# Performance work log

Measured on AMD Instinct MI355X. Metric: run time of the kernel, lower is better.

The kernel has to match this reference:

```python
import jax, jax.numpy as jnp
import numpy as np

NUM_HEADS = 16
D_MODEL = 1024


def setup_inputs() -> dict:
    key = jax.random.key(0)
    k1, k2, k3 = jax.random.split(key, 3)
    x = jax.random.normal(k1, (4, 2048, D_MODEL), dtype=jnp.float32)
    # torch.nn.Linear weights are [out_features, in_features]
    w_qkv = jax.random.normal(k2, (3 * D_MODEL, D_MODEL), dtype=jnp.float32) * (1.0 / np.sqrt(D_MODEL))
    w_o = jax.random.normal(k3, (D_MODEL, D_MODEL), dtype=jnp.float32) * (1.0 / np.sqrt(D_MODEL))
    return {"x": x, "w_qkv": w_qkv, "w_o": w_o}


def reference(x, w_qkv, w_o):
    b, n, _ = x.shape
    h = NUM_HEADS
    dh = D_MODEL // h  # head dim
    qkv = jnp.einsum('bnd,ed->bne', x, w_qkv)            # (b, n, 3*d_model)
    # Faithful to: rearrange(qkv, 'b n (h d) -> b h n d', h=h) then chunk(3, dim=-1)
    qkv = qkv.reshape(b, n, h, 3 * dh).transpose(0, 2, 1, 3)  # (b, h, n, 3*dh)
    q, k, v = jnp.split(qkv, 3, axis=-1)                 # each (b, h, n, dh)
    scale = 1.0 / jnp.sqrt(jnp.asarray(dh, dtype=x.dtype))
    scores = jnp.einsum('bhqd,bhkd->bhqk', q, k) * scale  # (b, h, n, n)
    attn = jax.nn.softmax(scores, axis=-1)
    out = jnp.einsum('bhqk,bhkd->bhqd', attn, v)          # (b, h, n, dh)
    out = out.transpose(0, 2, 1, 3).reshape(b, n, h * dh)  # 'b h n d -> b n (h d)'
    return jnp.einsum('bnd,ed->bne', out, w_o)
```

## Files before the change

### kernel.cpp

```cpp
#include <hip/hip_runtime.h>

#define BATCH 4
#define SEQ 2048
#define DM 1024
#define NH 16
#define DH 64
#define M_TOT (BATCH * SEQ)
#define EQKV (3 * DM)
#define QSCALE 0.18033688011112042f

typedef __bf16 bf16x8 __attribute__((ext_vector_type(8)));
typedef unsigned short u16x8 __attribute__((ext_vector_type(8)));
typedef float f32x2 __attribute__((ext_vector_type(2)));
typedef float f32x4 __attribute__((ext_vector_type(4)));
typedef float f32x16 __attribute__((ext_vector_type(16)));

static __device__ __forceinline__ unsigned short f2bf(float f) {
    unsigned int u = __builtin_bit_cast(unsigned int, f);
    u += 0x7fffu + ((u >> 16) & 1u);
    return (unsigned short)(u >> 16);
}

static __device__ __forceinline__ unsigned short f2bf_fast(float f) {
    return (unsigned short)((__builtin_bit_cast(unsigned int, f) + 0x8000u) >> 16);
}

static __device__ __forceinline__ unsigned int cvt_pk_bf16(float lo, float hi) {
    unsigned int r;
    asm("v_cvt_pk_bf16_f32 %0, %1, %2" : "=v"(r) : "v"(lo), "v"(hi));
    return r;
}

static __device__ __forceinline__ f32x2 pk_add(f32x2 a, f32x2 b) {
    f32x2 d;
    asm("v_pk_add_f32 %0, %1, %2" : "=v"(d) : "v"(a), "v"(b));
    return d;
}

static __device__ __forceinline__ float fast_exp2(float x) {
#if __has_builtin(__builtin_amdgcn_exp2f)
    return __builtin_amdgcn_exp2f(x);
#else
    return exp2f(x);
#endif
}

static __device__ __forceinline__ bf16x8 ld_frag(const ushort* p) {
    return *(const bf16x8*)p;
}

static __device__ __forceinline__ bf16x8 mk_frag(unsigned int a, unsigned int b,
                                                 unsigned int c, unsigned int d) {
    union { unsigned int u[4]; bf16x8 v; } t;
    t.u[0] = a; t.u[1] = b; t.u[2] = c; t.u[3] = d;
    return t.v;
}

static __device__ __forceinline__ void gload_lds16(const ushort* g, ushort* l) {
    __builtin_amdgcn_global_load_lds(
        (const __attribute__((address_space(1))) unsigned int*)g,
        (__attribute__((address_space(3))) unsigned int*)l,
        16, 0, 0);
}

#define BAR_TOP_COUNTED() do { \
        asm volatile("s_waitcnt vmcnt(4)" ::: "memory"); \
        __builtin_amdgcn_sched_barrier(0); \
        __builtin_amdgcn_s_barrier(); \
        __builtin_amdgcn_sched_barrier(0); \
    } while (0)
#define BAR_TOP_DRAIN() do { \
        asm volatile("s_waitcnt vmcnt(0)" ::: "memory"); \
        __builtin_amdgcn_sched_barrier(0); \
        __builtin_amdgcn_s_barrier(); \
        __builtin_amdgcn_sched_barrier(0); \
    } while (0)
#define BAR_END() do { \
        __builtin_amdgcn_sched_barrier(0); \
        asm volatile("s_waitcnt lgkmcnt(0)" ::: "memory"); \
        __builtin_amdgcn_s_barrier(); \
        __builtin_amdgcn_sched_barrier(0); \
    } while (0)

__global__ __launch_bounds__(256) void detect_kernel(const ushort* __restrict__ x,
                                                     int* __restrict__ flag) {
    __shared__ int cnt[256];
    const int tid = threadIdx.x;
    int c = 0;
    for (int j = 0; j < 16; ++j) {
        unsigned short w = x[tid * 16 + j];
        int e = (w >> 7) & 0xFF;
        bool sane = (e == 0) || (e >= 0x60 && e <= 0x8F);
        c += sane ? 0 : 1;
    }
    cnt[tid] = c;
    __syncthreads();
    for (int s = 128; s > 0; s >>= 1) {
        if (tid < s) cnt[tid] += cnt[tid + s];
        __syncthreads();
    }
    if (tid == 0) flag[0] = (cnt[0] > 256) ? 1 : 0;
}

__global__ __launch_bounds__(256) void convert_all_kernel(
    const void* __restrict__ xs, const void* __restrict__ wqs,
    const void* __restrict__ wos, ushort* __restrict__ XF,
    ushort* __restrict__ WQF, ushort* __restrict__ WOF,
    const int* __restrict__ flag)
{
    const int t = blockIdx.x * 256 + threadIdx.x;
    const int mg = t >> 7, kc = t & 127;

    const void* src;
    ushort* dst;
    int m;
    if (mg < M_TOT)            { src = xs;  dst = XF;  m = mg; }
    else if (mg < M_TOT + EQKV){ src = wqs; dst = WQF; m = mg - M_TOT; }
    else                       { src = wos; dst = WOF; m = mg - (M_TOT + EQKV); }

    u16x8 v;
    if (flag[0]) {
        const f32x4* s = (const f32x4*)((const float*)src + ((size_t)m * 128 + kc) * 8);
        const f32x4 lo = s[0], hi = s[1];
        #pragma unroll
        for (int j = 0; j < 4; ++j) v[j] = f2bf(lo[j]);
        #pragma unroll
        for (int j = 0; j < 4; ++j) v[4 + j] = f2bf(hi[j]);
    } else {
        v = *((const u16x8*)src + (size_t)m * 128 + kc);
    }
    const size_t o = (((size_t)(m >> 4) * 32 + (kc >> 2)) * 64 + (kc & 3) * 16 + (m & 15)) * 8;
    *(u16x8*)(dst + o) = v;
}

__global__ __launch_bounds__(256) void qkv_gemm_kernel(
    const ushort* __restrict__ XF, const ushort* __restrict__ WF,
    ushort* __restrict__ QF, ushort* __restrict__ KF, ushort* __restrict__ VF)
{
    __shared__ ushort As[2][8 * 512];
    __shared__ ushort Bs[2][8 * 512];

    const int lane = threadIdx.x & 63;
    const int wave = threadIdx.x >> 6;
    const int col  = lane & 15;
    const int quad = lane >> 4;
    const int orig = blockIdx.y * 24 + blockIdx.x;
    const int sid  = (orig & 7) * 192 + (orig >> 3);
    const int bx = sid % 24;
    const int by = sid / 24;
    const int m0 = by * 128 + (wave >> 1) * 64;
    const int e0 = bx * 128 + (wave & 1) * 64;
    const int mt0 = by * 8, et0 = bx * 8;
    const int wa = (wave >> 1) * 4;
    const int wb = (wave & 1) * 4;

    f32x4 acc[4][4];
    #pragma unroll
    for (int i = 0; i < 4; ++i)
        #pragma unroll
        for (int j = 0; j < 4; ++j) acc[i][j] = f32x4{0.f, 0.f, 0.f, 0.f};

#define GSTAGE(kt_, b_) do { \
        _Pragma("unroll") \
        for (int j_ = 0; j_ < 2; ++j_) { \
            const int c_ = wave * 2 + j_; \
            gload_lds16(XF + (size_t)((mt0 + c_) * 32 + (kt_)) * 512 + lane * 8, \
                        &As[b_][c_ * 512]); \
            gload_lds16(WF + (size_t)((et0 + c_) * 32 + (kt_)) * 512 + lane * 8, \
                        &Bs[b_][c_ * 512]); \
        } \
    } while (0)

    GSTAGE(0, 0);
    BAR_TOP_DRAIN();

    for (int kt = 0; kt < 32; ++kt) {
        const int cb = kt & 1;
        if (kt + 1 < 32) {
            GSTAGE(kt + 1, cb ^ 1);
            BAR_TOP_COUNTED();
        } else {
            BAR_TOP_DRAIN();
        }

        bf16x8 a[4], b[4];
        #pragma unroll
        for (int i = 0; i < 4; ++i) {
            a[i] = ld_frag(&As[cb][(wa + i) * 512] + lane * 8);
            b[i] = ld_frag(&Bs[cb][(wb + i) * 512] + lane * 8);
        }
        #pragma unroll
        for (int i = 0; i < 4; ++i)
            #pragma unroll
            for (int j = 0; j < 4; ++j)
                acc[i][j] = __builtin_amdgcn_mfma_f32_16x16x32_bf16(a[i], b[j], acc[i][j], 0, 0, 0);

        BAR_END();
    }
#undef GSTAGE

    #pragma unroll
    for (int ej = 0; ej < 4; ++ej) {
        const int e = e0 + ej * 16 + col;
        const int h = e / 192;
        const int c = e - h * 192;
        #pragma unroll
        for (int mi = 0; mi < 4; ++mi) {
            #pragma unroll
            for (int r = 0; r < 4; ++r) {
                const int m = m0 + mi * 16 + quad * 4 + r;
                const int bh = (m >> 11) * NH + h;
                const int n = m & (SEQ - 1);
                const float val = acc[mi][ej][r];
                if (c < 64) {
                    const int d = c;
                    QF[(((size_t)(bh * 64 + (n >> 5)) * 4 + (d >> 4)) * 64
                        + ((d >> 3) & 1) * 32 + (n & 31)) * 8 + (d & 7)] = f2bf_fast(val * QSCALE);
                } else if (c < 128) {
                    const int d = c - 64;
                    KF[(((size_t)(bh * 64 + (n >> 5)) * 4 + (d >> 4)) * 64
                        + ((d >> 3) & 1) * 32 + (n & 31)) * 8 + (d & 7)] = f2bf_fast(val);
                } else {
                    const int d = c - 128;
                    const int r4 = n & 15;
                    const int s4 = (r4 & 3) | (((r4 >> 3) & 1) << 2) | (((r4 >> 2) & 1) << 3);
                    VF[((((size_t)(bh * 32 + (n >> 6)) * 2 + (d >> 5)) * 4 + ((n >> 4) & 3)) * 64
                        + (s4 >> 3) * 32 + (d & 31)) * 8 + (s4 & 7)] = f2bf_fast(val);
                }
            }
        }
    }
}

__global__ __launch_bounds__(256) void attn_kernel(
    const ushort* __restrict__ QF, const ushort* __restrict__ KF,
    const ushort* __restrict__ VF, ushort* __restrict__ AOF)
{
    __shared__ ushort kvs[2][16 * 512];

    const int lane = threadIdx.x & 63;
    const int wave = threadIdx.x >> 6;
    const int half = lane >> 5;
    const int l31  = lane & 31;

    const int i = blockIdx.x;
    const int xcd = i & 7;
    const int s = i >> 3;
    const int qc = s & 15;
    const int bh = ((s >> 4) << 3) | xcd;
    const int q0 = qc * 128 + wave * 32;

    const ushort* qfb = QF + ((size_t)(bh * 64 + (q0 >> 5)) * 4) * 512;
    bf16x8 bq[4];
    #pragma unroll
    for (int d4 = 0; d4 < 4; ++d4) bq[d4] = ld_frag(qfb + d4 * 512 + lane * 8);

    const ushort* kfb = KF + (size_t)bh * 131072;
    const ushort* vfb = VF + (size_t)bh * 131072;

    f32x2 lp0 = {0.f, 0.f}, lp1 = {0.f, 0.f}, lp2 = {0.f, 0.f}, lp3 = {0.f, 0.f};
    f32x16 acc0 = {}, acc1 = {};

#define STAGE(it_, b_) do { \
        const size_t tb_ = (size_t)(it_) * 4096; \
        _Pragma("unroll") \
        for (int j_ = 0; j_ < 4; ++j_) { \
            const int f_ = wave * 4 + j_; \
            const ushort* src_ = (f_ < 8 ? kfb + tb_ + f_ * 512 \
                                         : vfb + tb_ + (f_ - 8) * 512) + lane * 8; \
            gload_lds16(src_, &kvs[b_][f_ * 512]); \
        } \
    } while (0)

#define LACC(v) do { \
        lp0 = pk_add(lp0, __builtin_shufflevector(v, v, 0, 1));   \
        lp1 = pk_add(lp1, __builtin_shufflevector(v, v, 2, 3));   \
        lp2 = pk_add(lp2, __builtin_shufflevector(v, v, 4, 5));   \
        lp3 = pk_add(lp3, __builtin_shufflevector(v, v, 6, 7));   \
        lp0 = pk_add(lp0, __builtin_shufflevector(v, v, 8, 9));   \
        lp1 = pk_add(lp1, __builtin_shufflevector(v, v, 10, 11)); \
        lp2 = pk_add(lp2, __builtin_shufflevector(v, v, 12, 13)); \
        lp3 = pk_add(lp3, __builtin_shufflevector(v, v, 14, 15)); \
    } while (0)

    STAGE(0, 0);
    BAR_TOP_DRAIN();

    for (int it = 0; it < 32; ++it) {
        const int cb = it & 1;
        if (it + 1 < 32) {
            STAGE(it + 1, cb ^ 1);
            BAR_TOP_COUNTED();
        } else {
            BAR_TOP_DRAIN();
        }

        const ushort* kp = &kvs[cb][0];

        f32x16 st0 = {}, st1 = {};
        #pragma unroll
        for (int d4 = 0; d4 < 4; ++d4) {
            bf16x8 ka0 = ld_frag(kp + d4 * 512 + lane * 8);
            bf16x8 ka1 = ld_frag(kp + (4 + d4) * 512 + lane * 8);
            st0 = __builtin_amdgcn_mfma_f32_32x32x16_bf16(ka0, bq[d4], st0, 0, 0, 0);
            st1 = __builtin_amdgcn_mfma_f32_32x32x16_bf16(ka1, bq[d4], st1, 0, 0, 0);
        }

        bf16x8 va0[4], va1[4];
        #pragma unroll
        for (int f4 = 0; f4 < 4; ++f4) {
            va0[f4] = ld_frag(kp + (8 + f4) * 512 + lane * 8);
            va1[f4] = ld_frag(kp + (12 + f4) * 512 + lane * 8);
        }

        #pragma unroll
        for (int t = 0; t < 16; ++t) st0[t] = fast_exp2(st0[t]);
        #pragma unroll
        for (int t = 0; t < 16; ++t) st1[t] = fast_exp2(st1[t]);
        LACC(st0);
        LACC(st1);

        bf16x8 pf[4];
        pf[0] = mk_frag(cvt_pk_bf16(st0[0],  st0[1]),  cvt_pk_bf16(st0[2],  st0[3]),
                        cvt_pk_bf16(st0[4],  st0[5]),  cvt_pk_bf16(st0[6],  st0[7]));
        pf[1] = mk_frag(cvt_pk_bf16(st0[8],  st0[9]),  cvt_pk_bf16(st0[10], st0[11]),
                        cvt_pk_bf16(st0[12], st0[13]), cvt_pk_bf16(st0[14], st0[15]));
        pf[2] = mk_frag(cvt_pk_bf16(st1[0],  st1[1]),  cvt_pk_bf16(st1[2],  st1[3]),
                        cvt_pk_bf16(st1[4],  st1[5]),  cvt_pk_bf16(st1[6],  st1[7]));
        pf[3] = mk_frag(cvt_pk_bf16(st1[8],  st1[9]),  cvt_pk_bf16(st1[10], st1[11]),
                        cvt_pk_bf16(st1[12], st1[13]), cvt_pk_bf16(st1[14], st1[15]));

        #pragma unroll
        for (int f4 = 0; f4 < 4; ++f4) {
            acc0 = __builtin_amdgcn_mfma_f32_32x32x16_bf16(va0[f4], pf[f4], acc0, 0, 0, 0);
            acc1 = __builtin_amdgcn_mfma_f32_32x32x16_bf16(va1[f4], pf[f4], acc1, 0, 0, 0);
        }

        BAR_END();
    }
#undef LACC
#undef STAGE

    f32x2 lt = pk_add(pk_add(lp0, lp1), pk_add(lp2, lp3));
    float l_i = lt[0] + lt[1];
    l_i += __shfl_xor(l_i, 32, 64);

    const int b = bh >> 4, h = bh & (NH - 1);
    const float inv = 1.f / l_i;
    const int n_g = b * SEQ + q0 + l31;
    #pragma unroll
    for (int r = 0; r < 16; ++r) {
        const int d = (r & 3) + 8 * (r >> 2) + 4 * half;
        #pragma unroll
        for (int p = 0; p < 2; ++p) {
            const int e = h * 64 + p * 32 + d;
            const float val = (p == 0 ? acc0[r] : acc1[r]) * inv;
            AOF[(((size_t)(n_g >> 4) * 32 + (e >> 5)) * 64
                 + ((e >> 3) & 3) * 16 + (n_g & 15)) * 8 + (e & 7)] = f2bf_fast(val);
        }
    }
}

__global__ __launch_bounds__(256) void out_gemm_kernel(
    const ushort* __restrict__ AOF, const ushort* __restrict__ WOF,
    void* __restrict__ out, const int* __restrict__ flag)
{
    __shared__ ushort As[2][8 * 512];
    __shared__ ushort Bs[2][8 * 512];

    const int lane = threadIdx.x & 63;
    const int wave = threadIdx.x >> 6;
    const int col  = lane & 15;
    const int quad = lane >> 4;
    const int orig = blockIdx.y * 8 + blockIdx.x;
    const int sid  = (orig & 7) * 64 + (orig >> 3);
    const int bx = sid & 7;
    const int by = sid >> 3;
    const int m0 = by * 128 + (wave >> 1) * 64;
    const int e0 = bx * 128 + (wave & 1) * 64;
    const int mt0 = by * 8, et0 = bx * 8;
    const int wa = (wave >> 1) * 4;
    const int wb = (wave & 1) * 4;
    const int f = flag[0];

    f32x4 acc[4][4];
    #pragma unroll
    for (int i = 0; i < 4; ++i)
        #pragma unroll
        for (int j = 0; j < 4; ++j) acc[i][j] = f32x4{0.f, 0.f, 0.f, 0.f};

#define GSTAGE(kt_, b_) do { \
        _Pragma("unroll") \
        for (int j_ = 0; j_ < 2; ++j_) { \
            const int c_ = wave * 2 + j_; \
            gload_lds16(AOF + (size_t)((mt0 + c_) * 32 + (kt_)) * 512 + lane * 8, \
                        &As[b_][c_ * 512]); \
            gload_lds16(WOF + (size_t)((et0 + c_) * 32 + (kt_)) * 512 + lane * 8, \
                        &Bs[b_][c_ * 512]); \
        } \
    } while (0)

    GSTAGE(0, 0);
    BAR_TOP_DRAIN();

    for (int kt = 0; kt < 32; ++kt) {
        const int cb = kt & 1;
        if (kt + 1 < 32) {
            GSTAGE(kt + 1, cb ^ 1);
            BAR_TOP_COUNTED();
        } else {
            BAR_TOP_DRAIN();
        }

        bf16x8 a[4], b[4];
        #pragma unroll
        for (int i = 0; i < 4; ++i) {
            a[i] = ld_frag(&As[cb][(wa + i) * 512] + lane * 8);
            b[i] = ld_frag(&Bs[cb][(wb + i) * 512] + lane * 8);
        }
        #pragma unroll
        for (int i = 0; i < 4; ++i)
            #pragma unroll
            for (int j = 0; j < 4; ++j)
                acc[i][j] = __builtin_amdgcn_mfma_f32_16x16x32_bf16(a[i], b[j], acc[i][j], 0, 0, 0);

        BAR_END();
    }
#undef GSTAGE

    if (f == 0) {
        ushort* o = (ushort*)out;
        #pragma unroll
        for (int mi = 0; mi < 4; ++mi)
            #pragma unroll
            for (int ej = 0; ej < 4; ++ej)
                #pragma unroll
                for (int r = 0; r < 4; ++r)
                    o[(size_t)(m0 + mi * 16 + quad * 4 + r) * DM + e0 + ej * 16 + col] = f2bf_fast(acc[mi][ej][r]);
    } else {
        float* o = (float*)out;
        #pragma unroll
        for (int mi = 0; mi < 4; ++mi)
            #pragma unroll
            for (int ej = 0; ej < 4; ++ej)
                #pragma unroll
                for (int r = 0; r < 4; ++r)
                    o[(size_t)(m0 + mi * 16 + quad * 4 + r) * DM + e0 + ej * 16 + col] = acc[mi][ej][r];
    }
}

extern "C" void kernel_launch(void* const* d_in, const int* in_sizes, int n_in,
                              void* d_out, int out_size, void* d_ws, size_t ws_size,
                              hipStream_t stream) {
    const void* x_raw     = d_in[0];
    const void* w_qkv_raw = d_in[1];
    const void* w_o_raw   = d_in[2];

    char* ws = (char*)d_ws;
    int*    flag  = (int*)ws;
    ushort* XF    = (ushort*)(ws + 256);
    ushort* WQKVF = (ushort*)(ws + 256 + (16u << 20));
    ushort* WOF   = (ushort*)(ws + 256 + (22u << 20));
    ushort* QF    = (ushort*)(ws + 256 + (24u << 20));
    ushort* KF    = (ushort*)(ws + 256 + (40u << 20));
    ushort* VF    = (ushort*)(ws + 256 + (56u << 20));
    ushort* AOF   = XF;

    detect_kernel<<<1, 256, 0, stream>>>((const ushort*)x_raw, flag);
    convert_all_kernel<<<(M_TOT + EQKV + DM) / 2, 256, 0, stream>>>(
        x_raw, w_qkv_raw, w_o_raw, XF, WQKVF, WOF, flag);

    qkv_gemm_kernel<<<dim3(EQKV / 128, M_TOT / 128), 256, 0, stream>>>(XF, WQKVF, QF, KF, VF);
    attn_kernel<<<dim3(BATCH * NH * (SEQ / 128)), 256, 0, stream>>>(QF, KF, VF, AOF);
    out_gemm_kernel<<<dim3(DM / 128, M_TOT / 128), 256, 0, stream>>>(AOF, WOF, d_out, flag);
}
```

Baseline: 295.6 us.

## Triple-buffer GEMM loads and compute softmax row sums with MFMA

Both projection GEMMs move from double to triple-buffered LDS staging, so loads run two k-tiles ahead and the wait counts are adjusted to match. In the attention kernel, the per-lane packed-add accumulation of the softmax denominator and the cross-lane shuffle are replaced by an extra MFMA per fragment against a vector of bf16 ones. This trades VALU work for matrix-core work, but the row sums now come from bf16-rounded probabilities rather than fp32 values. The GEMMs use more LDS, which may reduce occupancy.

```diff
diff --git a/kernel.cpp b/kernel.cpp
--- a/kernel.cpp
+++ b/kernel.cpp
@@ -11,7 +11,6 @@
 
 typedef __bf16 bf16x8 __attribute__((ext_vector_type(8)));
 typedef unsigned short u16x8 __attribute__((ext_vector_type(8)));
-typedef float f32x2 __attribute__((ext_vector_type(2)));
 typedef float f32x4 __attribute__((ext_vector_type(4)));
 typedef float f32x16 __attribute__((ext_vector_type(16)));
 
@@ -29,12 +28,6 @@
     unsigned int r;
     asm("v_cvt_pk_bf16_f32 %0, %1, %2" : "=v"(r) : "v"(lo), "v"(hi));
     return r;
-}
-
-static __device__ __forceinline__ f32x2 pk_add(f32x2 a, f32x2 b) {
-    f32x2 d;
-    asm("v_pk_add_f32 %0, %1, %2" : "=v"(d) : "v"(a), "v"(b));
-    return d;
 }
 
 static __device__ __forceinline__ float fast_exp2(float x) {
@@ -63,14 +56,8 @@
         16, 0, 0);
 }
 
-#define BAR_TOP_COUNTED() do { \
-        asm volatile("s_waitcnt vmcnt(4)" ::: "memory"); \
-        __builtin_amdgcn_sched_barrier(0); \
-        __builtin_amdgcn_s_barrier(); \
-        __builtin_amdgcn_sched_barrier(0); \
-    } while (0)
-#define BAR_TOP_DRAIN() do { \
-        asm volatile("s_waitcnt vmcnt(0)" ::: "memory"); \
+#define BAR_TOP(n_) do { \
+        asm volatile("s_waitcnt vmcnt(" #n_ ")" ::: "memory"); \
         __builtin_amdgcn_sched_barrier(0); \
         __builtin_amdgcn_s_barrier(); \
         __builtin_amdgcn_sched_barrier(0); \
@@ -137,8 +124,8 @@
     const ushort* __restrict__ XF, const ushort* __restrict__ WF,
     ushort* __restrict__ QF, ushort* __restrict__ KF, ushort* __restrict__ VF)
 {
-    __shared__ ushort As[2][8 * 512];
-    __shared__ ushort Bs[2][8 * 512];
+    __shared__ ushort As[3][8 * 512];
+    __shared__ ushort Bs[3][8 * 512];
 
     const int lane = threadIdx.x & 63;
     const int wave = threadIdx.x >> 6;
@@ -172,15 +159,17 @@
     } while (0)
 
     GSTAGE(0, 0);
-    BAR_TOP_DRAIN();
+    GSTAGE(1, 1);
 
     for (int kt = 0; kt < 32; ++kt) {
-        const int cb = kt & 1;
-        if (kt + 1 < 32) {
-            GSTAGE(kt + 1, cb ^ 1);
-            BAR_TOP_COUNTED();
+        const int cb = kt % 3;
+        if (kt + 2 < 32) {
+            GSTAGE(kt + 2, (kt + 2) % 3);
+            BAR_TOP(8);
+        } else if (kt == 30) {
+            BAR_TOP(4);
         } else {
-            BAR_TOP_DRAIN();
+            BAR_TOP(0);
         }
 
         bf16x8 a[4], b[4];
@@ -258,8 +247,9 @@
     const ushort* kfb = KF + (size_t)bh * 131072;
     const ushort* vfb = VF + (size_t)bh * 131072;
 
-    f32x2 lp0 = {0.f, 0.f}, lp1 = {0.f, 0.f}, lp2 = {0.f, 0.f}, lp3 = {0.f, 0.f};
+    const bf16x8 ones = mk_frag(0x3F803F80u, 0x3F803F80u, 0x3F803F80u, 0x3F803F80u);
     f32x16 acc0 = {}, acc1 = {};
+    f32x16 accl = {};
 
 #define STAGE(it_, b_) do { \
         const size_t tb_ = (size_t)(it_) * 4096; \
@@ -272,27 +262,16 @@
         } \
     } while (0)
 
-#define LACC(v) do { \
-        lp0 = pk_add(lp0, __builtin_shufflevector(v, v, 0, 1));   \
-        lp1 = pk_add(lp1, __builtin_shufflevector(v, v, 2, 3));   \
-        lp2 = pk_add(lp2, __builtin_shufflevector(v, v, 4, 5));   \
-        lp3 = pk_add(lp3, __builtin_shufflevector(v, v, 6, 7));   \
-        lp0 = pk_add(lp0, __builtin_shufflevector(v, v, 8, 9));   \
-        lp1 = pk_add(lp1, __builtin_shufflevector(v, v, 10, 11)); \
-        lp2 = pk_add(lp2, __builtin_shufflevector(v, v, 12, 13)); \
-        lp3 = pk_add(lp3, __builtin_shufflevector(v, v, 14, 15)); \
-    } while (0)
-
     STAGE(0, 0);
-    BAR_TOP_DRAIN();
+    BAR_TOP(0);
 
     for (int it = 0; it < 32; ++it) {
         const int cb = it & 1;
         if (it + 1 < 32) {
             STAGE(it + 1, cb ^ 1);
-            BAR_TOP_COUNTED();
+            BAR_TOP(4);
         } else {
-            BAR_TOP_DRAIN();
+            BAR_TOP(0);
         }
 
         const ushort* kp = &kvs[cb][0];
@@ -317,8 +296,6 @@
         for (int t = 0; t < 16; ++t) st0[t] = fast_exp2(st0[t]);
         #pragma unroll
         for (int t = 0; t < 16; ++t) st1[t] = fast_exp2(st1[t]);
-        LACC(st0);
-        LACC(st1);
 
         bf16x8 pf[4];
         pf[0] = mk_frag(cvt_pk_bf16(st0[0],  st0[1]),  cvt_pk_bf16(st0[2],  st0[3]),
@@ -334,16 +311,14 @@
         for (int f4 = 0; f4 < 4; ++f4) {
             acc0 = __builtin_amdgcn_mfma_f32_32x32x16_bf16(va0[f4], pf[f4], acc0, 0, 0, 0);
             acc1 = __builtin_amdgcn_mfma_f32_32x32x16_bf16(va1[f4], pf[f4], acc1, 0, 0, 0);
+            accl = __builtin_amdgcn_mfma_f32_32x32x16_bf16(ones,    pf[f4], accl, 0, 0, 0);
         }
 
         BAR_END();
     }
-#undef LACC
 #undef STAGE
 
-    f32x2 lt = pk_add(pk_add(lp0, lp1), pk_add(lp2, lp3));
-    float l_i = lt[0] + lt[1];
-    l_i += __shfl_xor(l_i, 32, 64);
+    const float l_i = accl[0];
 
     const int b = bh >> 4, h = bh & (NH - 1);
     const float inv = 1.f / l_i;
@@ -365,8 +340,8 @@
     const ushort* __restrict__ AOF, const ushort* __restrict__ WOF,
     void* __restrict__ out, const int* __restrict__ flag)
 {
-    __shared__ ushort As[2][8 * 512];
-    __shared__ ushort Bs[2][8 * 512];
+    __shared__ ushort As[3][8 * 512];
+    __shared__ ushort Bs[3][8 * 512];
 
     const int lane = threadIdx.x & 63;
     const int wave = threadIdx.x >> 6;
@@ -401,15 +376,17 @@
     } while (0)
 
     GSTAGE(0, 0);
-    BAR_TOP_DRAIN();
+    GSTAGE(1, 1);
 
     for (int kt = 0; kt < 32; ++kt) {
-        const int cb = kt & 1;
-        if (kt + 1 < 32) {
-            GSTAGE(kt + 1, cb ^ 1);
-            BAR_TOP_COUNTED();
+        const int cb = kt % 3;
+        if (kt + 2 < 32) {
+            GSTAGE(kt + 2, (kt + 2) % 3);
+            BAR_TOP(8);
+        } else if (kt == 30) {
+            BAR_TOP(4);
         } else {
-            BAR_TOP_DRAIN();
+            BAR_TOP(0);
         }
 
         bf16x8 a[4], b[4];
```

Measured after the change: 282.8 us, median of 3. 4.3% less time.
